# Kernel tuning notes

Measured on AMD Instinct MI355X. Metric: run time of the kernel, lower is better.

## Reference

```python
import jax, jax.numpy as jnp
import numpy as np

B, SQ, SKV, D, H = 2, 2048, 2048, 1024, 16
DH = D // H


def setup_inputs() -> dict:
    key = jax.random.key(0)
    ks = jax.random.split(key, 4)
    s = 0.02
    return {
        "query_input": jax.random.normal(ks[0], (B, SQ, D), jnp.float32),
        "kv_input": jax.random.normal(ks[1], (B, SKV, D), jnp.float32),
        "Wq": jax.random.normal(ks[2], (D, D), jnp.float32) * s,
        "bq": jnp.zeros((D,), jnp.float32),
        "Wkv": jax.random.normal(ks[3], (D, 2 * D), jnp.float32) * s,
        "bkv": jnp.zeros((2 * D,), jnp.float32),
        "Wo": jax.random.normal(jax.random.fold_in(key, 7), (D, D), jnp.float32) * s,
        "bo": jnp.zeros((D,), jnp.float32),
    }


def reference(query_input, kv_input, Wq, bq, Wkv, bkv, Wo, bo):
    scale = 1.0 / jnp.sqrt(jnp.float32(DH))
    # Projections
    q = query_input @ Wq + bq                      # [B, SQ, D]
    kv = kv_input @ Wkv + bkv                      # [B, SKV, 2D]
    k, v = jnp.split(kv, 2, axis=-1)               # [B, SKV, D] each
    # Split heads: [B, H, S, DH]
    q = q.reshape(B, SQ, H, DH).transpose(0, 2, 1, 3)
    k = k.reshape(B, SKV, H, DH).transpose(0, 2, 1, 3)
    v = v.reshape(B, SKV, H, DH).transpose(0, 2, 1, 3)
    # Scores S = QK^T / sqrt(d_k)
    scores = jnp.einsum("bhqd,bhkd->bhqk", q, k) * scale
    attn = jax.nn.softmax(scores, axis=-1)
    out = jnp.einsum("bhqk,bhkd->bhqd", attn, v)   # [B, H, SQ, DH]
    out = out.transpose(0, 2, 1, 3).reshape(B, SQ, D)
    return out @ Wo + bo
```

## Files before the change

### kernel.cpp

```cpp
#include <hip/hip_runtime.h>

typedef unsigned short u16;
typedef unsigned int u32;
typedef __bf16 bf16x8 __attribute__((ext_vector_type(8)));
typedef __bf16 bf16x2 __attribute__((ext_vector_type(2)));
typedef float f32x4 __attribute__((ext_vector_type(4)));
typedef float f32x16 __attribute__((ext_vector_type(16)));

#define QSCALE 0.18033688011112f

__device__ __forceinline__ u16 f2bf(float f) {
  u32 u = __builtin_bit_cast(u32, f);
  u += 0x7fffu + ((u >> 16) & 1u);
  return (u16)(u >> 16);
}

__device__ __forceinline__ u32 pkbf(float a, float b) {
  bf16x2 t = {(__bf16)a, (__bf16)b};
  return __builtin_bit_cast(u32, t);
}

__device__ __forceinline__ bf16x8 as_bf16x8(uint4 v) {
  return __builtin_bit_cast(bf16x8, v);
}

__device__ __forceinline__ void async16(const void* g, void* l) {
  __builtin_amdgcn_global_load_lds(
      (__attribute__((address_space(1))) void*)(g),
      (__attribute__((address_space(3))) void*)(l), 16, 0, 0);
}

__global__ void prep_kernel(const float* __restrict__ xq, const float* __restrict__ xkv,
                            const float* __restrict__ Wq, const float* __restrict__ Wkv,
                            const float* __restrict__ Wo,
                            u16* __restrict__ Xq16, u16* __restrict__ Xkv16,
                            u16* __restrict__ WqT, u16* __restrict__ WkvT,
                            u16* __restrict__ WoT) {
  const int bid = blockIdx.x, tid = threadIdx.x;
  if (bid < 8192) {
    int i = bid * 256 + tid;
    const float* s; u16* d; int j;
    if (i < 1048576) { s = xq; d = Xq16; j = i; }
    else             { s = xkv; d = Xkv16; j = i - 1048576; }
    float4 v = ((const float4*)s)[j];
    ushort4 o;
    o.x = f2bf(v.x); o.y = f2bf(v.y); o.z = f2bf(v.z); o.w = f2bf(v.w);
    ((ushort4*)d)[j] = o;
    return;
  }
  const int b2 = bid - 8192;
  const int z = b2 >> 11, rem = b2 & 2047;
  const int by = rem >> 6, bx = rem & 63;
  const float* src; u16* dst; int Nd;
  if (z == 0)      { src = Wq;  dst = WqT;  Nd = 1024; }
  else if (z == 1) { src = Wkv; dst = WkvT; Nd = 2048; }
  else             { src = Wo;  dst = WoT;  Nd = 1024; }
  const int n0 = bx * 32, k0 = by * 32;
  if (n0 >= Nd) return;
  __shared__ float tile[32][33];
  const int tx = tid & 31, ty = tid >> 5;
#pragma unroll
  for (int j = 0; j < 4; ++j)
    tile[ty + 8 * j][tx] = src[(size_t)(k0 + ty + 8 * j) * Nd + n0 + tx];
  __syncthreads();
#pragma unroll
  for (int j = 0; j < 4; ++j)
    dst[(size_t)(n0 + ty + 8 * j) * 1024 + k0 + tx] = f2bf(tile[tx][ty + 8 * j]);
}

template <int MI>
static __device__ __forceinline__ void gemm_core(
    const u16* __restrict__ A, const u16* __restrict__ Bt, int m0,
    uint4* sA, uint4* sB, f32x4 (*acc)[4]) {
  const int tid = threadIdx.x;
  const int wv = tid >> 6, lane = tid & 63;
  const int quad = lane >> 4, l16 = lane & 15;
  const int wm = (wv >> 1) * (MI * 16), wn = (wv & 1) * 64;

  const int ib0 = wv * 128 + lane, ib1 = ib0 + 64;
  const int br0 = ib0 >> 2, bc0 = (ib0 & 3) ^ ((br0 >> 1) & 3);
  const int br1 = ib1 >> 2, bc1 = (ib1 & 3) ^ ((br1 >> 1) & 3);
  const u16* gB0 = Bt + (size_t)br0 * 1024 + bc0 * 8;
  const u16* gB1 = Bt + (size_t)br1 * 1024 + bc1 * 8;

  const int ia0 = wv * (MI * 32) + lane;
  const int ar0 = ia0 >> 2, ac0 = (ia0 & 3) ^ ((ar0 >> 1) & 3);
  const u16* gA0 = A + (size_t)(m0 + ar0) * 1024 + ac0 * 8;
  const int ia1 = ia0 + 64;
  const int ar1 = ia1 >> 2, ac1 = (ia1 & 3) ^ ((ar1 >> 1) & 3);
  const u16* gA1 = A + (size_t)(m0 + ar1) * 1024 + ac1 * 8;
  uint4* sAw = sA + wv * (MI * 32);
  uint4* sBw = sB + wv * 128;

  for (int k0 = 0; k0 < 1024; k0 += 32) {
    __syncthreads();
    async16(gA0 + k0, sAw);
    if (MI == 4) async16(gA1 + k0, sAw + 64);
    async16(gB0 + k0, sBw);
    async16(gB1 + k0, sBw + 64);
    __syncthreads();

    bf16x8 af[MI], bfr[4];
#pragma unroll
    for (int mi = 0; mi < MI; ++mi) {
      int r = wm + mi * 16 + l16;
      af[mi] = as_bf16x8(sA[r * 4 + (quad ^ ((r >> 1) & 3))]);
    }
#pragma unroll
    for (int ni = 0; ni < 4; ++ni) {
      int r = wn + ni * 16 + l16;
      bfr[ni] = as_bf16x8(sB[r * 4 + (quad ^ ((r >> 1) & 3))]);
    }
#pragma unroll
    for (int mi = 0; mi < MI; ++mi)
#pragma unroll
      for (int ni = 0; ni < 4; ++ni)
        acc[mi][ni] = __builtin_amdgcn_mfma_f32_16x16x32_bf16(
            af[mi], bfr[ni], acc[mi][ni], 0, 0, 0);
  }
}

__global__ __launch_bounds__(256, 3) void gemm_qkv(
    const u16* __restrict__ Xq, const u16* __restrict__ Xkv,
    const u16* __restrict__ WqT, const u16* __restrict__ WkvT,
    const float* __restrict__ bq, const float* __restrict__ bkv,
    u16* __restrict__ Qd, u16* __restrict__ Kd, u16* __restrict__ Vd) {
  __shared__ uint4 sA[512], sB[512];
  f32x4 acc[4][4] = {};
  const int n0 = blockIdx.x * 128, m0 = blockIdx.y * 128;
  const u16* A = (n0 < 1024) ? Xq : Xkv;
  const u16* Bt = (n0 < 1024) ? (WqT + (size_t)n0 * 1024)
                              : (WkvT + (size_t)(n0 - 1024) * 1024);
  const float* bias = (n0 < 1024) ? (bq + n0) : (bkv + (n0 - 1024));
  gemm_core<4>(A, Bt, m0, sA, sB, acc);

  const int tid = threadIdx.x, wv = tid >> 6, lane = tid & 63;
  const int quad = lane >> 4, l16 = lane & 15;
  const int wm = (wv >> 1) * 64, wn = (wv & 1) * 64;
  const int bb = m0 >> 11;
  const int gmb = m0 + wm + quad * 4;
  const int ssb = (m0 & 2047) + wm + quad * 4;
#pragma unroll
  for (int ni = 0; ni < 4; ++ni) {
    const int gn = n0 + wn + ni * 16 + l16;
    const float bvn = bias[wn + ni * 16 + l16];
    if (gn < 1024) {
      u16* base = Qd + gn;
#pragma unroll
      for (int mi = 0; mi < 4; ++mi)
#pragma unroll
        for (int r = 0; r < 4; ++r)
          base[(size_t)(gmb + mi * 16 + r) * 1024] = f2bf((acc[mi][ni][r] + bvn) * QSCALE);
    } else if (gn < 2048) {
      u16* base = Kd + (gn - 1024);
#pragma unroll
      for (int mi = 0; mi < 4; ++mi)
#pragma unroll
        for (int r = 0; r < 4; ++r)
          base[(size_t)(gmb + mi * 16 + r) * 1024] = f2bf(acc[mi][ni][r] + bvn);
    } else {
      const int col = gn - 2048, hh = col >> 6, dh = col & 63;
      u16* base = Vd + ((size_t)(bb * 16 + hh) * 64 + dh) * 2048 + ssb;
#pragma unroll
      for (int mi = 0; mi < 4; ++mi) {
        ushort4 o;
        o.x = f2bf(acc[mi][ni][0] + bvn);
        o.y = f2bf(acc[mi][ni][1] + bvn);
        o.z = f2bf(acc[mi][ni][2] + bvn);
        o.w = f2bf(acc[mi][ni][3] + bvn);
        *(ushort4*)(base + mi * 16) = o;
      }
    }
  }
}

__global__ __launch_bounds__(512, 2) void flash_attn(
    const u16* __restrict__ Q, const u16* __restrict__ K,
    const u16* __restrict__ V, u16* __restrict__ O) {
  __shared__ uint4 sK[2][2][512];
  __shared__ uint4 sV[2][2][512];
  __shared__ float sO[16384];
  __shared__ float sLB[256];
  __shared__ float sLA[256];

  const int tid = threadIdx.x;
  const int wv = tid >> 6, lane = tid & 63;
  const int grp = wv >> 2, wq = wv & 3;
  const int c = lane & 31, hh = lane >> 5;
  const int hb = blockIdx.x & 31;
  const int q0 = (blockIdx.x >> 5) * 256;
  const int h = hb & 15, bz = hb >> 4;

  const u16* Qb = Q + ((size_t)(bz * 2048 + q0 + wq * 64)) * 1024 + h * 64;
  const u16* Kb = K + ((size_t)(bz * 2048 + grp * 64)) * 1024 + h * 64;
  const u16* Vb = V + ((size_t)(bz * 16 + h)) * 64 * 2048 + grp * 64;

  const int i0 = wq * 128 + lane, i1 = i0 + 64;
  const int r0 = i0 >> 3, r1 = i1 >> 3;
  const int ck0 = (i0 & 7) ^ (r0 & 7), ck1 = (i1 & 7) ^ (r1 & 7);
  const u16* gK0 = Kb + (size_t)r0 * 1024 + ck0 * 8;
  const u16* gK1 = Kb + (size_t)r1 * 1024 + ck1 * 8;
  const u16* gV0 = Vb + (size_t)r0 * 2048 + ck0 * 8;
  const u16* gV1 = Vb + (size_t)r1 * 2048 + ck1 * 8;
  const int wo = wq * 128;

  bf16x8 qf[2][4];
#pragma unroll
  for (int g = 0; g < 2; ++g) {
    const u16* qr = Qb + (size_t)(32 * g + c) * 1024 + hh * 8;
#pragma unroll
    for (int s = 0; s < 4; ++s)
      qf[g][s] = as_bf16x8(*(const uint4*)(qr + 16 * s));
  }

  f32x16 oacc[2][2] = {};
  float lp[2] = {0.f, 0.f};

  async16(gK0, &sK[grp][0][wo]);
  async16(gK1, &sK[grp][0][wo + 64]);
  async16(gV0, &sV[grp][0][wo]);
  async16(gV1, &sV[grp][0][wo + 64]);

  for (int t = 0; t < 16; ++t) {
    const int cur = t & 1;
    __syncthreads();
    if (t < 15) {
      const size_t ko = (size_t)(t + 1) * 128 * 1024;
      const int vo = (t + 1) * 128;
      async16(gK0 + ko, &sK[grp][cur ^ 1][wo]);
      async16(gK1 + ko, &sK[grp][cur ^ 1][wo + 64]);
      async16(gV0 + vo, &sV[grp][cur ^ 1][wo]);
      async16(gV1 + vo, &sV[grp][cur ^ 1][wo + 64]);
    }
    const uint4* K_ = sK[grp][cur];
    const uint4* V_ = sV[grp][cur];

    bf16x8 kf[2][4], vf[2][4];
#pragma unroll
    for (int b = 0; b < 2; ++b) {
      const int row = 32 * b + c, sw = row & 7;
#pragma unroll
      for (int s = 0; s < 4; ++s) {
        kf[b][s] = as_bf16x8(K_[row * 8 + ((2 * s + hh) ^ sw)]);
        vf[b][s] = as_bf16x8(V_[row * 8 + ((2 * s + hh) ^ sw)]);
      }
    }

    bf16x8 pa[2][4];
#pragma unroll
    for (int b = 0; b < 2; ++b)
#pragma unroll
      for (int g = 0; g < 2; ++g) {
        f32x16 sAcc = {};
#pragma unroll
        for (int s = 0; s < 4; ++s)
          sAcc = __builtin_amdgcn_mfma_f32_32x32x16_bf16(kf[b][s], qf[g][s], sAcc, 0, 0, 0);
        float e[16];
#pragma unroll
        for (int r = 0; r < 16; ++r) e[r] = __builtin_amdgcn_exp2f(sAcc[r]);
        float t0 = (e[0] + e[1]) + (e[2] + e[3]);
        float t1 = (e[4] + e[5]) + (e[6] + e[7]);
        float t2 = (e[8] + e[9]) + (e[10] + e[11]);
        float t3 = (e[12] + e[13]) + (e[14] + e[15]);
        lp[g] += (t0 + t1) + (t2 + t3);
        u32 wA0 = pkbf(e[0], e[1]),   wA1 = pkbf(e[2], e[3]);
        u32 wB0 = pkbf(e[4], e[5]),   wB1 = pkbf(e[6], e[7]);
        u32 wC0 = pkbf(e[8], e[9]),   wC1 = pkbf(e[10], e[11]);
        u32 wD0 = pkbf(e[12], e[13]), wD1 = pkbf(e[14], e[15]);
        asm("v_permlane32_swap_b32 %0, %1" : "+v"(wA0), "+v"(wB0));
        asm("v_permlane32_swap_b32 %0, %1" : "+v"(wA1), "+v"(wB1));
        asm("v_permlane32_swap_b32 %0, %1" : "+v"(wC0), "+v"(wD0));
        asm("v_permlane32_swap_b32 %0, %1" : "+v"(wC1), "+v"(wD1));
        uint4 f0 = {wA0, wA1, wB0, wB1};
        uint4 f1 = {wC0, wC1, wD0, wD1};
        pa[g][2 * b]     = as_bf16x8(f0);
        pa[g][2 * b + 1] = as_bf16x8(f1);
      }

#pragma unroll
    for (int g = 0; g < 2; ++g)
#pragma unroll
      for (int nb = 0; nb < 2; ++nb)
#pragma unroll
        for (int ks = 0; ks < 4; ++ks)
          oacc[g][nb] = __builtin_amdgcn_mfma_f32_32x32x16_bf16(
              pa[g][ks], vf[nb][ks], oacc[g][nb], 0, 0, 0);
  }

  float rtot[2];
#pragma unroll
  for (int g = 0; g < 2; ++g) {
    u32 a = __builtin_bit_cast(u32, lp[g]);
    u32 b = a;
    asm("v_permlane32_swap_b32 %0, %1" : "+v"(a), "+v"(b));
    rtot[g] = __builtin_bit_cast(float, a) + __builtin_bit_cast(float, b);
  }

  if (grp) {
#pragma unroll
    for (int g = 0; g < 2; ++g) {
      sLB[wq * 64 + 32 * g + c] = rtot[g];
#pragma unroll
      for (int nb = 0; nb < 2; ++nb) {
        float* dst = sO + (wq * 4 + g * 2 + nb) * 1024;
#pragma unroll
        for (int r = 0; r < 16; ++r)
          dst[r * 64 + lane] = oacc[g][nb][r];
      }
    }
  }
  __syncthreads();
  if (!grp) {
#pragma unroll
    for (int g = 0; g < 2; ++g) {
#pragma unroll
      for (int nb = 0; nb < 2; ++nb) {
        const float* srcp = sO + (wq * 4 + g * 2 + nb) * 1024;
#pragma unroll
        for (int r = 0; r < 16; ++r)
          oacc[g][nb][r] += srcp[r * 64 + lane];
      }
      float tot = rtot[g] + sLB[wq * 64 + 32 * g + c];
      sLA[wq * 64 + 32 * g + c] = 1.0f / tot;
    }
#pragma unroll
    for (int g = 0; g < 2; ++g) {
      u16* Ob = O + ((size_t)(bz * 2048 + q0 + wq * 64 + 32 * g)) * 1024 + h * 64;
#pragma unroll
      for (int nb = 0; nb < 2; ++nb)
#pragma unroll
        for (int r = 0; r < 16; ++r) {
          const int qr = (r & 3) + 8 * (r >> 2) + 4 * hh;
          float rl = sLA[wq * 64 + 32 * g + qr];
          Ob[(size_t)qr * 1024 + nb * 32 + c] = f2bf(oacc[g][nb][r] * rl);
        }
    }
  }
}

__global__ __launch_bounds__(256, 2) void gemm_out(
    const u16* __restrict__ A, const u16* __restrict__ Bt,
    const float* __restrict__ bias, float* __restrict__ C) {
  __shared__ uint4 sA[256], sB[512];
  f32x4 acc[2][4] = {};
  const int n0 = blockIdx.x * 128, m0 = blockIdx.y * 64;
  gemm_core<2>(A, Bt + (size_t)n0 * 1024, m0, sA, sB, acc);

  const int tid = threadIdx.x, wv = tid >> 6, lane = tid & 63;
  const int quad = lane >> 4, l16 = lane & 15;
  const int wm = (wv >> 1) * 32, wn = (wv & 1) * 64;
  float bv[4];
#pragma unroll
  for (int ni = 0; ni < 4; ++ni) bv[ni] = bias[n0 + wn + ni * 16 + l16];
#pragma unroll
  for (int mi = 0; mi < 2; ++mi)
#pragma unroll
    for (int ni = 0; ni < 4; ++ni)
#pragma unroll
      for (int r = 0; r < 4; ++r) {
        int gm = m0 + wm + mi * 16 + quad * 4 + r;
        int gn = n0 + wn + ni * 16 + l16;
        C[(size_t)gm * 1024 + gn] = acc[mi][ni][r] + bv[ni];
      }
}

extern "C" void kernel_launch(void* const* d_in, const int* in_sizes, int n_in,
                              void* d_out, int out_size, void* d_ws, size_t ws_size,
                              hipStream_t stream) {
  const float* xq  = (const float*)d_in[0];
  const float* xkv = (const float*)d_in[1];
  const float* Wq  = (const float*)d_in[2];
  const float* bq  = (const float*)d_in[3];
  const float* Wkv = (const float*)d_in[4];
  const float* bkv = (const float*)d_in[5];
  const float* Wo  = (const float*)d_in[6];
  const float* bo  = (const float*)d_in[7];
  float* out = (float*)d_out;

  char* p = (char*)d_ws;
  u16* Xq16  = (u16*)p; p += (size_t)8 << 20;
  u16* Xkv16 = (u16*)p; p += (size_t)8 << 20;
  u16* WqT   = (u16*)p; p += (size_t)2 << 20;
  u16* WkvT  = (u16*)p; p += (size_t)4 << 20;
  u16* WoT   = (u16*)p; p += (size_t)2 << 20;
  u16* Q16   = (u16*)p; p += (size_t)8 << 20;
  u16* K16   = (u16*)p; p += (size_t)8 << 20;
  u16* Vt16  = (u16*)p; p += (size_t)8 << 20;
  u16* O16   = (u16*)p; p += (size_t)8 << 20;

  prep_kernel<<<14336, 256, 0, stream>>>(xq, xkv, Wq, Wkv, Wo,
                                         Xq16, Xkv16, WqT, WkvT, WoT);
  gemm_qkv<<<dim3(24, 32), 256, 0, stream>>>(Xq16, Xkv16, WqT, WkvT, bq, bkv,
                                             Q16, K16, Vt16);
  flash_attn<<<256, 512, 0, stream>>>(Q16, K16, Vt16, O16);
  gemm_out<<<dim3(8, 64), 256, 0, stream>>>(O16, WoT, bo, out);
}
```

Measured before the change: 195.4 us.

## Split flash attention KV sweep across four wave groups with 1024-thread blocks

Doubles the flash-attention block to 1024 threads so four wave groups each process a quarter of the KV sequence, halving the per-group loop trips. The partial outputs and row sums are then merged through a reused shared buffer over several extra barrier stages. It also raises wave priority around the MFMA sequences with s_setprio. The cost is more reduction traffic and synchronisation at the end, plus higher register pressure from the launch bound of 1024 threads with min 4 blocks.

```diff
diff --git a/kernel.cpp b/kernel.cpp
--- a/kernel.cpp
+++ b/kernel.cpp
@@ -174,13 +174,11 @@
   }
 }
 
-__global__ __launch_bounds__(512, 2) void flash_attn(
+__global__ __launch_bounds__(1024, 4) void flash_attn(
     const u16* __restrict__ Q, const u16* __restrict__ K,
     const u16* __restrict__ V, u16* __restrict__ O) {
-  __shared__ uint4 sK[2][2][512];
-  __shared__ uint4 sV[2][2][512];
-  __shared__ float sO[16384];
-  __shared__ float sLB[256];
+  __shared__ uint4 sbuf[8192];
+  __shared__ float sLB[4][256];
   __shared__ float sLA[256];
 
   const int tid = threadIdx.x;
@@ -194,6 +192,9 @@
   const u16* Qb = Q + ((size_t)(bz * 2048 + q0 + wq * 64)) * 1024 + h * 64;
   const u16* Kb = K + ((size_t)(bz * 2048 + grp * 64)) * 1024 + h * 64;
   const u16* Vb = V + ((size_t)(bz * 16 + h)) * 64 * 2048 + grp * 64;
+
+  uint4* sKg = sbuf + grp * 1024;
+  uint4* sVg = sbuf + 4096 + grp * 1024;
 
   const int i0 = wq * 128 + lane, i1 = i0 + 64;
   const int r0 = i0 >> 3, r1 = i1 >> 3;
@@ -216,24 +217,24 @@
   f32x16 oacc[2][2] = {};
   float lp[2] = {0.f, 0.f};
 
-  async16(gK0, &sK[grp][0][wo]);
-  async16(gK1, &sK[grp][0][wo + 64]);
-  async16(gV0, &sV[grp][0][wo]);
-  async16(gV1, &sV[grp][0][wo + 64]);
-
-  for (int t = 0; t < 16; ++t) {
+  async16(gK0, sKg + wo);
+  async16(gK1, sKg + wo + 64);
+  async16(gV0, sVg + wo);
+  async16(gV1, sVg + wo + 64);
+
+  for (int t = 0; t < 8; ++t) {
     const int cur = t & 1;
     __syncthreads();
-    if (t < 15) {
-      const size_t ko = (size_t)(t + 1) * 128 * 1024;
-      const int vo = (t + 1) * 128;
-      async16(gK0 + ko, &sK[grp][cur ^ 1][wo]);
-      async16(gK1 + ko, &sK[grp][cur ^ 1][wo + 64]);
-      async16(gV0 + vo, &sV[grp][cur ^ 1][wo]);
-      async16(gV1 + vo, &sV[grp][cur ^ 1][wo + 64]);
-    }
-    const uint4* K_ = sK[grp][cur];
-    const uint4* V_ = sV[grp][cur];
+    if (t < 7) {
+      const size_t ko = (size_t)(t + 1) * 256 * 1024;
+      const int vo = (t + 1) * 256;
+      async16(gK0 + ko, sKg + (cur ^ 1) * 512 + wo);
+      async16(gK1 + ko, sKg + (cur ^ 1) * 512 + wo + 64);
+      async16(gV0 + vo, sVg + (cur ^ 1) * 512 + wo);
+      async16(gV1 + vo, sVg + (cur ^ 1) * 512 + wo + 64);
+    }
+    const uint4* K_ = sKg + cur * 512;
+    const uint4* V_ = sVg + cur * 512;
 
     bf16x8 kf[2][4], vf[2][4];
 #pragma unroll
@@ -252,9 +253,11 @@
 #pragma unroll
       for (int g = 0; g < 2; ++g) {
         f32x16 sAcc = {};
+        __builtin_amdgcn_s_setprio(1);
 #pragma unroll
         for (int s = 0; s < 4; ++s)
           sAcc = __builtin_amdgcn_mfma_f32_32x32x16_bf16(kf[b][s], qf[g][s], sAcc, 0, 0, 0);
+        __builtin_amdgcn_s_setprio(0);
         float e[16];
 #pragma unroll
         for (int r = 0; r < 16; ++r) e[r] = __builtin_amdgcn_exp2f(sAcc[r]);
@@ -277,6 +280,7 @@
         pa[g][2 * b + 1] = as_bf16x8(f1);
       }
 
+    __builtin_amdgcn_s_setprio(1);
 #pragma unroll
     for (int g = 0; g < 2; ++g)
 #pragma unroll
@@ -285,6 +289,7 @@
         for (int ks = 0; ks < 4; ++ks)
           oacc[g][nb] = __builtin_amdgcn_mfma_f32_32x32x16_bf16(
               pa[g][ks], vf[nb][ks], oacc[g][nb], 0, 0, 0);
+    __builtin_amdgcn_s_setprio(0);
   }
 
   float rtot[2];
@@ -294,34 +299,63 @@
     u32 b = a;
     asm("v_permlane32_swap_b32 %0, %1" : "+v"(a), "+v"(b));
     rtot[g] = __builtin_bit_cast(float, a) + __builtin_bit_cast(float, b);
-  }
-
-  if (grp) {
-#pragma unroll
-    for (int g = 0; g < 2; ++g) {
-      sLB[wq * 64 + 32 * g + c] = rtot[g];
+    sLB[grp][wq * 64 + 32 * g + c] = rtot[g];
+  }
+
+  __syncthreads();
+  float* scr = (float*)sbuf;
+
+  if (grp == 1 || grp == 2) {
+#pragma unroll
+    for (int g = 0; g < 2; ++g)
 #pragma unroll
       for (int nb = 0; nb < 2; ++nb) {
-        float* dst = sO + (wq * 4 + g * 2 + nb) * 1024;
+        float* dst = scr + ((((grp - 1) * 4 + wq) * 4) + g * 2 + nb) * 1024;
 #pragma unroll
         for (int r = 0; r < 16; ++r)
           dst[r * 64 + lane] = oacc[g][nb][r];
       }
-    }
   }
   __syncthreads();
-  if (!grp) {
+  if (grp == 0) {
+#pragma unroll
+    for (int src = 0; src < 2; ++src)
+#pragma unroll
+      for (int g = 0; g < 2; ++g)
+#pragma unroll
+        for (int nb = 0; nb < 2; ++nb) {
+          const float* sp = scr + (((src * 4 + wq) * 4) + g * 2 + nb) * 1024;
+#pragma unroll
+          for (int r = 0; r < 16; ++r)
+            oacc[g][nb][r] += sp[r * 64 + lane];
+        }
+  }
+  __syncthreads();
+  if (grp == 3) {
+#pragma unroll
+    for (int g = 0; g < 2; ++g)
+#pragma unroll
+      for (int nb = 0; nb < 2; ++nb) {
+        float* dst = scr + ((wq * 4) + g * 2 + nb) * 1024;
+#pragma unroll
+        for (int r = 0; r < 16; ++r)
+          dst[r * 64 + lane] = oacc[g][nb][r];
+      }
+  }
+  __syncthreads();
+  if (grp == 0) {
 #pragma unroll
     for (int g = 0; g < 2; ++g) {
 #pragma unroll
       for (int nb = 0; nb < 2; ++nb) {
-        const float* srcp = sO + (wq * 4 + g * 2 + nb) * 1024;
+        const float* sp = scr + ((wq * 4) + g * 2 + nb) * 1024;
 #pragma unroll
         for (int r = 0; r < 16; ++r)
-          oacc[g][nb][r] += srcp[r * 64 + lane];
-      }
-      float tot = rtot[g] + sLB[wq * 64 + 32 * g + c];
-      sLA[wq * 64 + 32 * g + c] = 1.0f / tot;
+          oacc[g][nb][r] += sp[r * 64 + lane];
+      }
+      const int li = wq * 64 + 32 * g + c;
+      float tot = rtot[g] + sLB[1][li] + sLB[2][li] + sLB[3][li];
+      sLA[li] = 1.0f / tot;
     }
 #pragma unroll
     for (int g = 0; g < 2; ++g) {
@@ -392,6 +426,6 @@
                                          Xq16, Xkv16, WqT, WkvT, WoT);
   gemm_qkv<<<dim3(24, 32), 256, 0, stream>>>(Xq16, Xkv16, WqT, WkvT, bq, bkv,
                                              Q16, K16, Vt16);
-  flash_attn<<<256, 512, 0, stream>>>(Q16, K16, Vt16, O16);
+  flash_attn<<<256, 1024, 0, stream>>>(Q16, K16, Vt16, O16);
   gemm_out<<<dim3(8, 64), 256, 0, stream>>>(O16, WoT, bo, out);
 }
```

Result: slower. 481.5 us (+146.4%).

## Halve flash-attn query tile per block, alias LDS buffers, add MFMA priority

Applied to the files above, without the earlier changes.

Each wave now handles 32 query rows instead of 64, and the grid doubles to 512 blocks with launch bounds of 4 blocks per CU. The K/V staging buffers and the cross-group output reduction scratch now share one LDS array, which cuts shared memory so more blocks fit per CU. V fragment loads move after the softmax, and s_setprio wraps the MFMA sections. The aim is higher occupancy and better latency hiding, at the cost of loading each K/V tile twice as often per query row and fewer MFMAs per LDS read.

```diff
diff --git a/kernel.cpp b/kernel.cpp
--- a/kernel.cpp
+++ b/kernel.cpp
@@ -174,26 +174,27 @@
   }
 }
 
-__global__ __launch_bounds__(512, 2) void flash_attn(
+__global__ __launch_bounds__(512, 4) void flash_attn(
     const u16* __restrict__ Q, const u16* __restrict__ K,
     const u16* __restrict__ V, u16* __restrict__ O) {
-  __shared__ uint4 sK[2][2][512];
-  __shared__ uint4 sV[2][2][512];
-  __shared__ float sO[16384];
-  __shared__ float sLB[256];
-  __shared__ float sLA[256];
+  __shared__ uint4 sbuf[4096];
+  __shared__ float sLB[128];
+  __shared__ float sLA[128];
 
   const int tid = threadIdx.x;
   const int wv = tid >> 6, lane = tid & 63;
   const int grp = wv >> 2, wq = wv & 3;
   const int c = lane & 31, hh = lane >> 5;
   const int hb = blockIdx.x & 31;
-  const int q0 = (blockIdx.x >> 5) * 256;
+  const int q0 = (blockIdx.x >> 5) * 128;
   const int h = hb & 15, bz = hb >> 4;
 
-  const u16* Qb = Q + ((size_t)(bz * 2048 + q0 + wq * 64)) * 1024 + h * 64;
+  const u16* Qb = Q + ((size_t)(bz * 2048 + q0 + wq * 32)) * 1024 + h * 64;
   const u16* Kb = K + ((size_t)(bz * 2048 + grp * 64)) * 1024 + h * 64;
   const u16* Vb = V + ((size_t)(bz * 16 + h)) * 64 * 2048 + grp * 64;
+
+  uint4* sKg = sbuf + grp * 1024;
+  uint4* sVg = sbuf + 2048 + grp * 1024;
 
   const int i0 = wq * 128 + lane, i1 = i0 + 64;
   const int r0 = i0 >> 3, r1 = i1 >> 3;
@@ -204,22 +205,21 @@
   const u16* gV1 = Vb + (size_t)r1 * 2048 + ck1 * 8;
   const int wo = wq * 128;
 
-  bf16x8 qf[2][4];
-#pragma unroll
-  for (int g = 0; g < 2; ++g) {
-    const u16* qr = Qb + (size_t)(32 * g + c) * 1024 + hh * 8;
+  bf16x8 qf[4];
+  {
+    const u16* qr = Qb + (size_t)c * 1024 + hh * 8;
 #pragma unroll
     for (int s = 0; s < 4; ++s)
-      qf[g][s] = as_bf16x8(*(const uint4*)(qr + 16 * s));
-  }
-
-  f32x16 oacc[2][2] = {};
-  float lp[2] = {0.f, 0.f};
-
-  async16(gK0, &sK[grp][0][wo]);
-  async16(gK1, &sK[grp][0][wo + 64]);
-  async16(gV0, &sV[grp][0][wo]);
-  async16(gV1, &sV[grp][0][wo + 64]);
+      qf[s] = as_bf16x8(*(const uint4*)(qr + 16 * s));
+  }
+
+  f32x16 oacc[2] = {};
+  float lp = 0.f;
+
+  async16(gK0, sKg + wo);
+  async16(gK1, sKg + wo + 64);
+  async16(gV0, sVg + wo);
+  async16(gV1, sVg + wo + 64);
 
   for (int t = 0; t < 16; ++t) {
     const int cur = t & 1;
@@ -227,114 +227,115 @@
     if (t < 15) {
       const size_t ko = (size_t)(t + 1) * 128 * 1024;
       const int vo = (t + 1) * 128;
-      async16(gK0 + ko, &sK[grp][cur ^ 1][wo]);
-      async16(gK1 + ko, &sK[grp][cur ^ 1][wo + 64]);
-      async16(gV0 + vo, &sV[grp][cur ^ 1][wo]);
-      async16(gV1 + vo, &sV[grp][cur ^ 1][wo + 64]);
-    }
-    const uint4* K_ = sK[grp][cur];
-    const uint4* V_ = sV[grp][cur];
-
-    bf16x8 kf[2][4], vf[2][4];
+      async16(gK0 + ko, sKg + (cur ^ 1) * 512 + wo);
+      async16(gK1 + ko, sKg + (cur ^ 1) * 512 + wo + 64);
+      async16(gV0 + vo, sVg + (cur ^ 1) * 512 + wo);
+      async16(gV1 + vo, sVg + (cur ^ 1) * 512 + wo + 64);
+    }
+    const uint4* K_ = sKg + cur * 512;
+    const uint4* V_ = sVg + cur * 512;
+
+    bf16x8 kf[2][4];
 #pragma unroll
     for (int b = 0; b < 2; ++b) {
       const int row = 32 * b + c, sw = row & 7;
 #pragma unroll
-      for (int s = 0; s < 4; ++s) {
+      for (int s = 0; s < 4; ++s)
         kf[b][s] = as_bf16x8(K_[row * 8 + ((2 * s + hh) ^ sw)]);
-        vf[b][s] = as_bf16x8(V_[row * 8 + ((2 * s + hh) ^ sw)]);
-      }
-    }
-
-    bf16x8 pa[2][4];
-#pragma unroll
-    for (int b = 0; b < 2; ++b)
-#pragma unroll
-      for (int g = 0; g < 2; ++g) {
-        f32x16 sAcc = {};
-#pragma unroll
-        for (int s = 0; s < 4; ++s)
-          sAcc = __builtin_amdgcn_mfma_f32_32x32x16_bf16(kf[b][s], qf[g][s], sAcc, 0, 0, 0);
-        float e[16];
-#pragma unroll
-        for (int r = 0; r < 16; ++r) e[r] = __builtin_amdgcn_exp2f(sAcc[r]);
-        float t0 = (e[0] + e[1]) + (e[2] + e[3]);
-        float t1 = (e[4] + e[5]) + (e[6] + e[7]);
-        float t2 = (e[8] + e[9]) + (e[10] + e[11]);
-        float t3 = (e[12] + e[13]) + (e[14] + e[15]);
-        lp[g] += (t0 + t1) + (t2 + t3);
-        u32 wA0 = pkbf(e[0], e[1]),   wA1 = pkbf(e[2], e[3]);
-        u32 wB0 = pkbf(e[4], e[5]),   wB1 = pkbf(e[6], e[7]);
-        u32 wC0 = pkbf(e[8], e[9]),   wC1 = pkbf(e[10], e[11]);
-        u32 wD0 = pkbf(e[12], e[13]), wD1 = pkbf(e[14], e[15]);
-        asm("v_permlane32_swap_b32 %0, %1" : "+v"(wA0), "+v"(wB0));
-        asm("v_permlane32_swap_b32 %0, %1" : "+v"(wA1), "+v"(wB1));
-        asm("v_permlane32_swap_b32 %0, %1" : "+v"(wC0), "+v"(wD0));
-        asm("v_permlane32_swap_b32 %0, %1" : "+v"(wC1), "+v"(wD1));
-        uint4 f0 = {wA0, wA1, wB0, wB1};
-        uint4 f1 = {wC0, wC1, wD0, wD1};
-        pa[g][2 * b]     = as_bf16x8(f0);
-        pa[g][2 * b + 1] = as_bf16x8(f1);
-      }
-
-#pragma unroll
-    for (int g = 0; g < 2; ++g)
-#pragma unroll
-      for (int nb = 0; nb < 2; ++nb)
-#pragma unroll
-        for (int ks = 0; ks < 4; ++ks)
-          oacc[g][nb] = __builtin_amdgcn_mfma_f32_32x32x16_bf16(
-              pa[g][ks], vf[nb][ks], oacc[g][nb], 0, 0, 0);
-  }
-
-  float rtot[2];
-#pragma unroll
-  for (int g = 0; g < 2; ++g) {
-    u32 a = __builtin_bit_cast(u32, lp[g]);
+    }
+
+    bf16x8 pa[4];
+#pragma unroll
+    for (int b = 0; b < 2; ++b) {
+      f32x16 sAcc = {};
+      __builtin_amdgcn_s_setprio(1);
+#pragma unroll
+      for (int s = 0; s < 4; ++s)
+        sAcc = __builtin_amdgcn_mfma_f32_32x32x16_bf16(kf[b][s], qf[s], sAcc, 0, 0, 0);
+      __builtin_amdgcn_s_setprio(0);
+      float e[16];
+#pragma unroll
+      for (int r = 0; r < 16; ++r) e[r] = __builtin_amdgcn_exp2f(sAcc[r]);
+      float t0 = (e[0] + e[1]) + (e[2] + e[3]);
+      float t1 = (e[4] + e[5]) + (e[6] + e[7]);
+      float t2 = (e[8] + e[9]) + (e[10] + e[11]);
+      float t3 = (e[12] + e[13]) + (e[14] + e[15]);
+      lp += (t0 + t1) + (t2 + t3);
+      u32 wA0 = pkbf(e[0], e[1]),   wA1 = pkbf(e[2], e[3]);
+      u32 wB0 = pkbf(e[4], e[5]),   wB1 = pkbf(e[6], e[7]);
+      u32 wC0 = pkbf(e[8], e[9]),   wC1 = pkbf(e[10], e[11]);
+      u32 wD0 = pkbf(e[12], e[13]), wD1 = pkbf(e[14], e[15]);
+      asm("v_permlane32_swap_b32 %0, %1" : "+v"(wA0), "+v"(wB0));
+      asm("v_permlane32_swap_b32 %0, %1" : "+v"(wA1), "+v"(wB1));
+      asm("v_permlane32_swap_b32 %0, %1" : "+v"(wC0), "+v"(wD0));
+      asm("v_permlane32_swap_b32 %0, %1" : "+v"(wC1), "+v"(wD1));
+      uint4 f0 = {wA0, wA1, wB0, wB1};
+      uint4 f1 = {wC0, wC1, wD0, wD1};
+      pa[2 * b]     = as_bf16x8(f0);
+      pa[2 * b + 1] = as_bf16x8(f1);
+    }
+
+    bf16x8 vf[2][4];
+#pragma unroll
+    for (int nb = 0; nb < 2; ++nb) {
+      const int row = 32 * nb + c, sw = row & 7;
+#pragma unroll
+      for (int ks = 0; ks < 4; ++ks)
+        vf[nb][ks] = as_bf16x8(V_[row * 8 + ((2 * ks + hh) ^ sw)]);
+    }
+
+    __builtin_amdgcn_s_setprio(1);
+#pragma unroll
+    for (int nb = 0; nb < 2; ++nb)
+#pragma unroll
+      for (int ks = 0; ks < 4; ++ks)
+        oacc[nb] = __builtin_amdgcn_mfma_f32_32x32x16_bf16(
+            pa[ks], vf[nb][ks], oacc[nb], 0, 0, 0);
+    __builtin_amdgcn_s_setprio(0);
+  }
+
+  float rtot;
+  {
+    u32 a = __builtin_bit_cast(u32, lp);
     u32 b = a;
     asm("v_permlane32_swap_b32 %0, %1" : "+v"(a), "+v"(b));
-    rtot[g] = __builtin_bit_cast(float, a) + __builtin_bit_cast(float, b);
-  }
+    rtot = __builtin_bit_cast(float, a) + __builtin_bit_cast(float, b);
+  }
+  if (grp) sLB[wq * 32 + c] = rtot;
+
+  __syncthreads();
+  float* scr = (float*)sbuf;
 
   if (grp) {
 #pragma unroll
-    for (int g = 0; g < 2; ++g) {
-      sLB[wq * 64 + 32 * g + c] = rtot[g];
-#pragma unroll
-      for (int nb = 0; nb < 2; ++nb) {
-        float* dst = sO + (wq * 4 + g * 2 + nb) * 1024;
-#pragma unroll
-        for (int r = 0; r < 16; ++r)
-          dst[r * 64 + lane] = oacc[g][nb][r];
-      }
+    for (int nb = 0; nb < 2; ++nb) {
+      float* dst = scr + (wq * 2 + nb) * 1024;
+#pragma unroll
+      for (int r = 0; r < 16; ++r)
+        dst[r * 64 + lane] = oacc[nb][r];
     }
   }
   __syncthreads();
   if (!grp) {
 #pragma unroll
-    for (int g = 0; g < 2; ++g) {
-#pragma unroll
-      for (int nb = 0; nb < 2; ++nb) {
-        const float* srcp = sO + (wq * 4 + g * 2 + nb) * 1024;
-#pragma unroll
-        for (int r = 0; r < 16; ++r)
-          oacc[g][nb][r] += srcp[r * 64 + lane];
+    for (int nb = 0; nb < 2; ++nb) {
+      const float* sp = scr + (wq * 2 + nb) * 1024;
+#pragma unroll
+      for (int r = 0; r < 16; ++r)
+        oacc[nb][r] += sp[r * 64 + lane];
+    }
+    float tot = rtot + sLB[wq * 32 + c];
+    sLA[wq * 32 + c] = 1.0f / tot;
+
+    u16* Ob = O + ((size_t)(bz * 2048 + q0 + wq * 32)) * 1024 + h * 64;
+#pragma unroll
+    for (int nb = 0; nb < 2; ++nb)
+#pragma unroll
+      for (int r = 0; r < 16; ++r) {
+        const int qr = (r & 3) + 8 * (r >> 2) + 4 * hh;
+        float rl = sLA[wq * 32 + qr];
+        Ob[(size_t)qr * 1024 + nb * 32 + c] = f2bf(oacc[nb][r] * rl);
       }
-      float tot = rtot[g] + sLB[wq * 64 + 32 * g + c];
-      sLA[wq * 64 + 32 * g + c] = 1.0f / tot;
-    }
-#pragma unroll
-    for (int g = 0; g < 2; ++g) {
-      u16* Ob = O + ((size_t)(bz * 2048 + q0 + wq * 64 + 32 * g)) * 1024 + h * 64;
-#pragma unroll
-      for (int nb = 0; nb < 2; ++nb)
-#pragma unroll
-        for (int r = 0; r < 16; ++r) {
-          const int qr = (r & 3) + 8 * (r >> 2) + 4 * hh;
-          float rl = sLA[wq * 64 + 32 * g + qr];
-          Ob[(size_t)qr * 1024 + nb * 32 + c] = f2bf(oacc[g][nb][r] * rl);
-        }
-    }
   }
 }
 
@@ -392,6 +393,6 @@
                                          Xq16, Xkv16, WqT, WkvT, WoT);
   gemm_qkv<<<dim3(24, 32), 256, 0, stream>>>(Xq16, Xkv16, WqT, WkvT, bq, bkv,
                                              Q16, K16, Vt16);
-  flash_attn<<<256, 512, 0, stream>>>(Q16, K16, Vt16, O16);
+  flash_attn<<<512, 512, 0, stream>>>(Q16, K16, Vt16, O16);
   gemm_out<<<dim3(8, 64), 256, 0, stream>>>(O16, WoT, bo, out);
 }
```

Measured after the change: 196.4 us. Within noise of the previous version (+0.5%).
